# Optimization experiments

Measured on AMD Instinct MI355X. Metric: run time of the kernel, lower is better.

The kernel has to match this reference:

```python
import jax, jax.numpy as jnp
import numpy as np

DIM = 2048
HEADS = 16
HEAD_DIM = DIM // HEADS
B, S = 2, 2048


def setup_inputs() -> dict:
    key = jax.random.key(0)
    k1, k2, k3 = jax.random.split(key, 3)
    x = jax.random.normal(k1, (B, S, DIM), dtype=jnp.float32)
    # causal mask (True = keep), realistic production usage of masked_fill(mask==0,...)
    mask = jnp.tril(jnp.ones((S, S), dtype=bool))
    scale = 1.0 / np.sqrt(DIM)
    W_qkv = jax.random.normal(k2, (DIM, 3 * DIM), dtype=jnp.float32) * scale
    b_qkv = jnp.zeros((3 * DIM,), dtype=jnp.float32)
    W_out = jax.random.normal(k3, (DIM, DIM), dtype=jnp.float32) * scale
    b_out = jnp.zeros((DIM,), dtype=jnp.float32)
    return {"x": x, "mask": mask, "W_qkv": W_qkv, "b_qkv": b_qkv,
            "W_out": W_out, "b_out": b_out}


def reference(x, mask, W_qkv, b_qkv, W_out, b_out):
    b, s, d = x.shape
    # fused QKV projection: [b,s,3d]
    qkv = jnp.einsum('bsd,de->bse', x, W_qkv) + b_qkv
    # [b, s, h, 3*hd] -> [b, h, s, 3*hd] -> chunk into q,k,v
    qkv = qkv.reshape(b, s, HEADS, 3 * HEAD_DIM).transpose(0, 2, 1, 3)
    q, k, v = jnp.split(qkv, 3, axis=-1)  # each [b,h,s,hd]
    scores = jnp.einsum('bhqd,bhkd->bhqk', q, k) / np.sqrt(HEAD_DIM)
    scores = jnp.where(mask, scores, jnp.float32(-1e9))
    attn = jax.nn.softmax(scores, axis=-1)
    # dropout_rate = 0.0 (eval) -> identity
    out = jnp.einsum('bhqk,bhkd->bhqd', attn, v)  # [b,h,s,hd]
    out = out.transpose(0, 2, 1, 3).reshape(b, s, d)
    return jnp.einsum('bsd,de->bse', out, W_out) + b_out
```

## Files before the change

kernel.cpp:

```cpp
#include <hip/hip_runtime.h>
#include <hip/hip_bf16.h>

#define SEQ   2048
#define DIMSZ 2048
#define NHEAD 16
#define HD    128
#define KDIM  2048

typedef __attribute__((ext_vector_type(8))) short bf16x8;
typedef __attribute__((ext_vector_type(4))) float f32x4;
typedef __attribute__((ext_vector_type(4))) short short4v;
typedef __attribute__((ext_vector_type(4))) float float4v;

__device__ __forceinline__ short f2bf(float f) {
    union { __hip_bfloat16 h; short s; } u;
    u.h = __float2bfloat16(f);
    return u.s;
}

__device__ __forceinline__ void gload_lds16(const void* g, void* l) {
    __builtin_amdgcn_global_load_lds(
        (const __attribute__((address_space(1))) void*)g,
        (__attribute__((address_space(3))) void*)l, 16, 0, 0);
}

__global__ __launch_bounds__(256) void cvt_bf16(const float* __restrict__ in,
                                                short* __restrict__ out) {
    int i = (blockIdx.x * 256 + threadIdx.x) * 4;
    float4v v = *reinterpret_cast<const float4v*>(in + i);
    short4v o;
    o[0] = f2bf(v[0]); o[1] = f2bf(v[1]); o[2] = f2bf(v[2]); o[3] = f2bf(v[3]);
    *reinterpret_cast<short4v*>(out + i) = o;
}

__global__ __launch_bounds__(256) void transpose_cvt(const float* __restrict__ in,
                                                     short* __restrict__ out,
                                                     int R, int C) {
    __shared__ float tile[32][33];
    int c0 = blockIdx.x * 32, r0 = blockIdx.y * 32;
    int tx = threadIdx.x, ty = threadIdx.y;
#pragma unroll
    for (int i = 0; i < 32; i += 8)
        tile[ty + i][tx] = in[(long)(r0 + ty + i) * C + c0 + tx];
    __syncthreads();
#pragma unroll
    for (int i = 0; i < 32; i += 8)
        out[(long)(c0 + ty + i) * R + r0 + tx] = f2bf(tile[tx][ty + i]);
}

template <int MODE, int BM, int BN, int WMC, int WNC>
__global__ __launch_bounds__(512, 2) void gemm8p(const short* __restrict__ A,
                                                 const short* __restrict__ Bt,
                                                 const float* __restrict__ bias,
                                                 float* __restrict__ outf,
                                                 short* __restrict__ q_buf,
                                                 short* __restrict__ k_buf,
                                                 short* __restrict__ vt_buf,
                                                 int ntx) {
    constexpr int QMW = (BM / 2) / WMC;
    constexpr int QNW = (BN / 2) / WNC;
    constexpr int MA = QMW / 16;
    constexpr int NB = QNW / 16;
    constexpr int UA = BM / 64, UB = BN / 64, UT = UA + UB;
    constexpr int RA = MA * 2, RB = NB * 2;
    constexpr int BH0C = (BN / 2 + 63) / 64;
    constexpr int NE = UA / 2 + BH0C, NL = UT - NE;
    constexpr int S0 = 2, S2 = 2;
    constexpr int VM0 = NE + S0;
    constexpr int VM2 = NL + S2;
    constexpr int VM3 = (NE - S2) + NE;
    constexpr int NT = KDIM / 64;

    __shared__ __align__(16) short Alds[2][BM * 64];
    __shared__ __align__(16) short Blds[2][BN * 64];

    const int tid = threadIdx.x;
    const int wv = tid >> 6, ln = tid & 63;
    const int lr = ln & 15, lg = ln >> 4;
    const int wm = wv / WNC, wn = wv % WNC;
    const int q8 = gridDim.x >> 3;
    const int id = blockIdx.x;
    const int swz = (id & 7) * q8 + (id >> 3);
    const int m0 = (swz / ntx) * BM, n0 = (swz % ntx) * BN;

    const int r_l = wv * 8 + (ln >> 3);
    const int g8 = ((ln & 7) ^ ((ln >> 3) & 7)) << 3;

#define STAGE_U(u, bufi, TT)                                                   \
    {                                                                          \
        const bool isA_ = (u) < UA / 2 || (u) >= UA / 2 + UB;                  \
        const int idx_ = (u) < UA / 2 ? (u)                                    \
                         : ((u) < UA / 2 + UB ? (u) - UA / 2 : (u) - UB);      \
        if (isA_)                                                              \
            gload_lds16(A + (long)(m0 + idx_ * 64 + r_l) * KDIM + (TT)*64 + g8,\
                        &Alds[bufi][idx_ * 4096 + wv * 512]);                  \
        else                                                                   \
            gload_lds16(Bt + (long)(n0 + idx_ * 64 + r_l) * KDIM + (TT)*64 + g8,\
                        &Blds[bufi][idx_ * 4096 + wv * 512]);                  \
    }

#define RD(L_, row_, kk_) \
    (*reinterpret_cast<const bf16x8*>(&(L_)[(row_)*64 + ((((kk_)*4 + lg) ^ ((row_)&7)) << 3)]))

#define RD_A(bufi, mh, bank)                                                   \
    _Pragma("unroll") for (int mi = 0; mi < MA; ++mi) {                        \
        int r_ = (mh) * (BM / 2) + wm * QMW + mi * 16 + lr;                    \
        bank[mi][0] = RD(Alds[bufi], r_, 0);                                   \
        bank[mi][1] = RD(Alds[bufi], r_, 1);                                   \
    }
#define RD_B(bufi, nh, bank)                                                   \
    _Pragma("unroll") for (int ni = 0; ni < NB; ++ni) {                        \
        int r_ = (nh) * (BN / 2) + wn * QNW + ni * 16 + lr;                    \
        bank[ni][0] = RD(Blds[bufi], r_, 0);                                   \
        bank[ni][1] = RD(Blds[bufi], r_, 1);                                   \
    }

#define MFMA_Q(qi, AB, BB)                                                     \
    __builtin_amdgcn_s_setprio(1);                                             \
    _Pragma("unroll") for (int kk = 0; kk < 2; ++kk)                           \
        _Pragma("unroll") for (int mi = 0; mi < MA; ++mi)                      \
            _Pragma("unroll") for (int ni = 0; ni < NB; ++ni)                  \
                acc[qi][mi][ni] = __builtin_amdgcn_mfma_f32_16x16x32_bf16(     \
                    AB[mi][kk], BB[ni][kk], acc[qi][mi][ni], 0, 0, 0);         \
    __builtin_amdgcn_s_setprio(0);

#define LGKM(n)                                                                \
    asm volatile("s_waitcnt lgkmcnt(%0)" ::"i"(n) : "memory");                 \
    __builtin_amdgcn_sched_barrier(0);
#define VMC(n) asm volatile("s_waitcnt vmcnt(%0)" ::"i"(n) : "memory");
#define BAR()                                                                  \
    __builtin_amdgcn_s_barrier();                                              \
    __builtin_amdgcn_sched_barrier(0);

    f32x4 acc[4][MA][NB] = {};
    bf16x8 aF0[MA][2], aF1[MA][2], bF0a[NB][2], bF0b[NB][2], bF1[NB][2];

#pragma unroll
    for (int u = 0; u < UT; ++u) STAGE_U(u, 0, 0);
#pragma unroll
    for (int u = 0; u < NE; ++u) STAGE_U(u, 1, 1);
    VMC(NE);
    BAR();
    RD_A(0, 0, aF0);
    RD_B(0, 0, bF0a);

#define TILE_BODY(PAR, T_, BF0C, BF0N)                                         \
    {                                                                          \
        constexpr int cur = PAR, nxt = PAR ^ 1;                                \
                 \
        RD_B(cur, 1, bF1);                                                     \
        if ((T_) + 1 < NT) {                                                   \
            STAGE_U(NE + 0, nxt, (T_) + 1);                                    \
            STAGE_U(NE + 1, nxt, (T_) + 1);                                    \
        }                                                                      \
        LGKM(RB);                                                              \
        MFMA_Q(0, aF0, BF0C);                                                  \
        VMC(VM0);                                                              \
        BAR();                                                                 \
                \
        RD_A(cur, 1, aF1);                                                     \
        if ((T_) + 1 < NT) {                                                   \
            _Pragma("unroll") for (int u = NE + S0; u < UT; ++u)               \
                STAGE_U(u, nxt, (T_) + 1);                                     \
        }                                                                      \
        LGKM(RA);                                                              \
        MFMA_Q(1, aF0, bF1);                                                   \
        BAR();                                                                 \
                       \
        if ((T_) + 2 < NT) {                                                   \
            STAGE_U(0, cur, (T_) + 2);                                         \
            STAGE_U(1, cur, (T_) + 2);                                         \
        }                                                                      \
        LGKM(0);                                                               \
        MFMA_Q(2, aF1, bF1);                                                   \
        if ((T_) + 2 < NT) { VMC(VM2); } else { VMC(NL); }                     \
        BAR();                                                                 \
           \
        if ((T_) + 1 < NT) {                                                   \
            RD_A(nxt, 0, aF0);                                                 \
            RD_B(nxt, 0, BF0N);                                                \
        }                                                                      \
        if ((T_) + 2 < NT) {                                                   \
            _Pragma("unroll") for (int u = S2; u < NE; ++u)                    \
                STAGE_U(u, cur, (T_) + 2);                                     \
        }                                                                      \
        LGKM(RA + RB);                                                         \
        MFMA_Q(3, aF1, BF0C);                                                  \
        if ((T_) + 2 < NT) { VMC(VM3); } else { VMC(0); }                      \
        BAR();                                                                 \
    }

    for (int TT = 0; TT < NT; TT += 2) {
        TILE_BODY(0, TT, bF0a, bF0b);
        TILE_BODY(1, TT + 1, bF0b, bF0a);
    }

    const int MH[4] = {0, 0, 1, 1}, NHq[4] = {0, 1, 1, 0};
#pragma unroll
    for (int q = 0; q < 4; ++q) {
#pragma unroll
        for (int mi = 0; mi < MA; ++mi) {
#pragma unroll
            for (int ni = 0; ni < NB; ++ni) {
                int col = n0 + NHq[q] * (BN / 2) + wn * QNW + ni * 16 + lr;
                float bv = bias[col];
#pragma unroll
                for (int j = 0; j < 4; ++j) {
                    int row = m0 + MH[q] * (BM / 2) + wm * QMW + mi * 16 + lg * 4 + j;
                    float v = acc[q][mi][ni][j] + bv;
                    if (MODE == 0) {
                        int h = col / (3 * HD);
                        int jj = col - h * (3 * HD);
                        int b = row >> 11, s = row & 2047;
                        int bh = b * NHEAD + h;
                        short sv = f2bf(v);
                        if (jj < HD)
                            q_buf[(bh * SEQ + s) * HD + jj] = sv;
                        else if (jj < 2 * HD)
                            k_buf[(bh * SEQ + s) * HD + (jj - HD)] = sv;
                        else
                            vt_buf[(bh * HD + (jj - 2 * HD)) * SEQ + s] = sv;
                    } else {
                        outf[(long)row * DIMSZ + col] = v;
                    }
                }
            }
        }
    }
#undef STAGE_U
#undef RD
#undef RD_A
#undef RD_B
#undef MFMA_Q
#undef LGKM
#undef VMC
#undef BAR
#undef TILE_BODY
}

__global__ __launch_bounds__(256, 2) void attn_kernel(const short* __restrict__ q_buf,
                                                      const short* __restrict__ k_buf,
                                                      const short* __restrict__ vt_buf,
                                                      short* __restrict__ ao) {
    __shared__ __align__(16) short Klds[2][64 * 128];
    __shared__ __align__(16) short Vlds[2][128 * 64];
    __shared__ __align__(16) short Plds[4][32 * 64];
    const int tid = threadIdx.x;
    const int wave = tid >> 6, lane = tid & 63;
    const int lr = lane & 15, lg = lane >> 4;
    const int bx = blockIdx.x;
    const int qt = 15 - (bx >> 5);
    const int bh = bx & 31;
    const int b = bh >> 4, h = bh & 15;
    const int qbase = qt * 128 + wave * 32;
    const float scale = 0.08838834764831845f;

    bf16x8 qf[2][4];
    {
        const short* qrow = q_buf + ((long)(bh * SEQ + qbase + lr)) * HD;
#pragma unroll
        for (int mi = 0; mi < 2; ++mi)
#pragma unroll
            for (int c = 0; c < 4; ++c)
                qf[mi][c] = *reinterpret_cast<const bf16x8*>(
                    qrow + mi * 16 * HD + c * 32 + lg * 8);
    }
    asm volatile("s_waitcnt vmcnt(0)" ::: "memory");

    const char* kbase = (const char*)(k_buf + (long)bh * SEQ * HD);
    const char* vbase = (const char*)(vt_buf + (long)bh * HD * SEQ);
    const int krow_l = wave * 4 + (lane >> 4);
    const int kcol_l = ((lane & 15) * 16) ^ ((krow_l & 7) << 4);
    const int vrow_l = wave * 8 + (lane >> 3);
    const int vcol_l = ((lane & 7) * 16) ^ ((vrow_l & 7) << 4);

    const int nt = 2 * (qt + 1);
    auto stage = [&](int bufi, int t) {
        const char* ks = kbase + (long)t * 16384 + (long)krow_l * 256 + kcol_l;
        const char* vs = vbase + (long)t * 128 + (long)vrow_l * (SEQ * 2) + vcol_l;
        short* kd = &Klds[bufi][wave * 512];
        short* vd = &Vlds[bufi][wave * 512];
#pragma unroll
        for (int i = 0; i < 4; ++i) {
            gload_lds16(ks + i * 4096, kd + i * 2048);
            gload_lds16(vs + (long)i * 32 * SEQ * 2, vd + i * 2048);
        }
    };

    f32x4 o_acc[2][8] = {};
    float mrow[2][4], lrow[2][4];
#pragma unroll
    for (int mi = 0; mi < 2; ++mi)
#pragma unroll
        for (int j = 0; j < 4; ++j) { mrow[mi][j] = -1e30f; lrow[mi][j] = 0.f; }
    short* pw = &Plds[wave][0];

    stage(0, 0);
    for (int t = 0; t < nt; ++t) {
        const int cur = t & 1;
        if (t + 1 < nt) {
            stage(cur ^ 1, t + 1);
            asm volatile("s_waitcnt vmcnt(8)" ::: "memory");
        } else {
            asm volatile("s_waitcnt vmcnt(0)" ::: "memory");
        }
        __builtin_amdgcn_s_barrier();
        __builtin_amdgcn_sched_barrier(0);

        const int kv0 = t * 64;
        if (kv0 <= qbase + 31) {
            f32x4 sc[2][4] = {};
            const short* kl = &Klds[cur][0];
#pragma unroll
            for (int c = 0; c < 4; ++c) {
                bf16x8 kf[4];
#pragma unroll
                for (int ni = 0; ni < 4; ++ni)
                    kf[ni] = *reinterpret_cast<const bf16x8*>(
                        kl + (((ni * 16 + lr) * 256 +
                               ((c * 64 + lg * 16) ^ ((lr & 7) << 4))) >> 1));
#pragma unroll
                for (int mi = 0; mi < 2; ++mi)
#pragma unroll
                    for (int ni = 0; ni < 4; ++ni)
                        sc[mi][ni] = __builtin_amdgcn_mfma_f32_16x16x32_bf16(
                            qf[mi][c], kf[ni], sc[mi][ni], 0, 0, 0);
            }
            const bool full = (kv0 + 63) <= qbase;
            float pv[2][4][4], pm[2][4];
#pragma unroll
            for (int mi = 0; mi < 2; ++mi)
#pragma unroll
                for (int j = 0; j < 4; ++j) {
                    float mx = -3e38f;
#pragma unroll
                    for (int ni = 0; ni < 4; ++ni) {
                        float v = sc[mi][ni][j] * scale;
                        if (!full) {
                            int qg = qbase + mi * 16 + lg * 4 + j;
                            if (kv0 + ni * 16 + lr > qg) v = -1e9f;
                        }
                        pv[mi][ni][j] = v;
                        mx = fmaxf(mx, v);
                    }
                    pm[mi][j] = mx;
                }
#pragma unroll
            for (int m = 1; m < 16; m <<= 1)
#pragma unroll
                for (int mi = 0; mi < 2; ++mi)
#pragma unroll
                    for (int j = 0; j < 4; ++j)
                        pm[mi][j] = fmaxf(pm[mi][j], __shfl_xor(pm[mi][j], m, 64));
            float alpha[2][4], psum[2][4];
#pragma unroll
            for (int mi = 0; mi < 2; ++mi)
#pragma unroll
                for (int j = 0; j < 4; ++j) {
                    float mn = fmaxf(mrow[mi][j], pm[mi][j]);
                    alpha[mi][j] = __expf(mrow[mi][j] - mn);
                    mrow[mi][j] = mn;
                    psum[mi][j] = 0.f;
                }
#pragma unroll
            for (int mi = 0; mi < 2; ++mi)
#pragma unroll
                for (int ni = 0; ni < 4; ++ni)
#pragma unroll
                    for (int j = 0; j < 4; ++j) {
                        float p = __expf(pv[mi][ni][j] - mrow[mi][j]);
                        pv[mi][ni][j] = p;
                        psum[mi][j] += p;
                    }
#pragma unroll
            for (int m = 1; m < 16; m <<= 1)
#pragma unroll
                for (int mi = 0; mi < 2; ++mi)
#pragma unroll
                    for (int j = 0; j < 4; ++j)
                        psum[mi][j] += __shfl_xor(psum[mi][j], m, 64);
#pragma unroll
            for (int mi = 0; mi < 2; ++mi)
#pragma unroll
                for (int j = 0; j < 4; ++j)
                    lrow[mi][j] = lrow[mi][j] * alpha[mi][j] + psum[mi][j];
#pragma unroll
            for (int mi = 0; mi < 2; ++mi)
#pragma unroll
                for (int n = 0; n < 8; ++n)
#pragma unroll
                    for (int j = 0; j < 4; ++j)
                        o_acc[mi][n][j] *= alpha[mi][j];
#pragma unroll
            for (int mi = 0; mi < 2; ++mi)
#pragma unroll
                for (int ni = 0; ni < 4; ++ni)
#pragma unroll
                    for (int j = 0; j < 4; ++j) {
                        int row = mi * 16 + lg * 4 + j;
                        int cb = (ni * 32 + lr * 2) ^ ((row & 7) << 4);
                        pw[(row * 128 + cb) >> 1] = f2bf(pv[mi][ni][j]);
                    }
            const short* vl = &Vlds[cur][0];
#pragma unroll
            for (int kc = 0; kc < 2; ++kc) {
                bf16x8 pa[2];
#pragma unroll
                for (int mi = 0; mi < 2; ++mi)
                    pa[mi] = *reinterpret_cast<const bf16x8*>(
                        pw + (((mi * 16 + lr) * 128 +
                               ((kc * 64 + lg * 16) ^ ((lr & 7) << 4))) >> 1));
#pragma unroll
                for (int n = 0; n < 8; ++n) {
                    bf16x8 vf = *reinterpret_cast<const bf16x8*>(
                        vl + (((n * 16 + lr) * 128 +
                               ((kc * 64 + lg * 16) ^ ((lr & 7) << 4))) >> 1));
#pragma unroll
                    for (int mi = 0; mi < 2; ++mi)
                        o_acc[mi][n] = __builtin_amdgcn_mfma_f32_16x16x32_bf16(
                            pa[mi], vf, o_acc[mi][n], 0, 0, 0);
                }
            }
        }
        __builtin_amdgcn_s_barrier();
    }

    float inv[2][4];
#pragma unroll
    for (int mi = 0; mi < 2; ++mi)
#pragma unroll
        for (int j = 0; j < 4; ++j) inv[mi][j] = 1.0f / lrow[mi][j];
    short* aor = ao + ((long)(b * SEQ + qbase) * DIMSZ + h * HD);
#pragma unroll
    for (int mi = 0; mi < 2; ++mi)
#pragma unroll
        for (int n = 0; n < 8; ++n)
#pragma unroll
            for (int j = 0; j < 4; ++j)
                aor[(mi * 16 + lg * 4 + j) * DIMSZ + n * 16 + lr] =
                    f2bf(o_acc[mi][n][j] * inv[mi][j]);
}

extern "C" void kernel_launch(void* const* d_in, const int* in_sizes, int n_in,
                              void* d_out, int out_size, void* d_ws, size_t ws_size,
                              hipStream_t stream) {
    const float* x     = (const float*)d_in[0];
    const float* W_qkv = (const float*)d_in[2];
    const float* b_qkv = (const float*)d_in[3];
    const float* W_out = (const float*)d_in[4];
    const float* b_out = (const float*)d_in[5];
    float* out = (float*)d_out;

    char* ws = (char*)d_ws;
    short* x_bf   = (short*)ws;
    short* wqkv_t = (short*)(ws + (size_t)16 * 1048576);
    short* wout_t = (short*)(ws + (size_t)40 * 1048576);
    short* q_buf  = (short*)(ws + (size_t)48 * 1048576);
    short* k_buf  = (short*)(ws + (size_t)64 * 1048576);
    short* vt_buf = (short*)(ws + (size_t)80 * 1048576);
    short* ao     = x_bf;

    cvt_bf16<<<8192, 256, 0, stream>>>(x, x_bf);
    transpose_cvt<<<dim3(192, 64), dim3(32, 8), 0, stream>>>(W_qkv, wqkv_t, 2048, 6144);
    transpose_cvt<<<dim3(64, 64), dim3(32, 8), 0, stream>>>(W_out, wout_t, 2048, 2048);
    gemm8p<0, 256, 192, 4, 2><<<512, 512, 0, stream>>>(x_bf, wqkv_t, b_qkv, nullptr,
                                                       q_buf, k_buf, vt_buf, 32);
    attn_kernel<<<512, 256, 0, stream>>>(q_buf, k_buf, vt_buf, ao);
    gemm8p<1, 128, 256, 2, 4><<<256, 512, 0, stream>>>(ao, wout_t, b_out, out,
                                                       nullptr, nullptr, nullptr, 8);
}
```

Baseline: 327.8 us.

## Restructure attention into single-wave blocks reading K/V directly from global

```diff
diff --git a/kernel.cpp b/kernel.cpp
--- a/kernel.cpp
+++ b/kernel.cpp
@@ -147,7 +147,6 @@
 #define TILE_BODY(PAR, T_, BF0C, BF0N)                                         \
     {                                                                          \
         constexpr int cur = PAR, nxt = PAR ^ 1;                                \
-                 \
         RD_B(cur, 1, bF1);                                                     \
         if ((T_) + 1 < NT) {                                                   \
             STAGE_U(NE + 0, nxt, (T_) + 1);                                    \
@@ -157,7 +156,6 @@
         MFMA_Q(0, aF0, BF0C);                                                  \
         VMC(VM0);                                                              \
         BAR();                                                                 \
-                \
         RD_A(cur, 1, aF1);                                                     \
         if ((T_) + 1 < NT) {                                                   \
             _Pragma("unroll") for (int u = NE + S0; u < UT; ++u)               \
@@ -166,7 +164,6 @@
         LGKM(RA);                                                              \
         MFMA_Q(1, aF0, bF1);                                                   \
         BAR();                                                                 \
-                       \
         if ((T_) + 2 < NT) {                                                   \
             STAGE_U(0, cur, (T_) + 2);                                         \
             STAGE_U(1, cur, (T_) + 2);                                         \
@@ -175,7 +172,6 @@
         MFMA_Q(2, aF1, bF1);                                                   \
         if ((T_) + 2 < NT) { VMC(VM2); } else { VMC(NL); }                     \
         BAR();                                                                 \
-           \
         if ((T_) + 1 < NT) {                                                   \
             RD_A(nxt, 0, aF0);                                                 \
             RD_B(nxt, 0, BF0N);                                                \
@@ -238,21 +234,19 @@
 #undef TILE_BODY
 }
 
-__global__ __launch_bounds__(256, 2) void attn_kernel(const short* __restrict__ q_buf,
-                                                      const short* __restrict__ k_buf,
-                                                      const short* __restrict__ vt_buf,
-                                                      short* __restrict__ ao) {
-    __shared__ __align__(16) short Klds[2][64 * 128];
-    __shared__ __align__(16) short Vlds[2][128 * 64];
-    __shared__ __align__(16) short Plds[4][32 * 64];
-    const int tid = threadIdx.x;
-    const int wave = tid >> 6, lane = tid & 63;
+__global__ __launch_bounds__(64, 3) void attn_kernel(const short* __restrict__ q_buf,
+                                                     const short* __restrict__ k_buf,
+                                                     const short* __restrict__ vt_buf,
+                                                     short* __restrict__ ao) {
+    __shared__ __align__(16) short Plds[32 * 64];
+    const int lane = threadIdx.x;
     const int lr = lane & 15, lg = lane >> 4;
     const int bx = blockIdx.x;
-    const int qt = 15 - (bx >> 5);
-    const int bh = bx & 31;
+    const int t = (bx & 7) * 256 + (bx >> 3);
+    const int bh = t >> 6;
+    const int qt = 63 - (t & 63);
     const int b = bh >> 4, h = bh & 15;
-    const int qbase = qt * 128 + wave * 32;
+    const int qbase = qt * 32;
     const float scale = 0.08838834764831845f;
 
     bf16x8 qf[2][4];
@@ -265,27 +259,9 @@
                 qf[mi][c] = *reinterpret_cast<const bf16x8*>(
                     qrow + mi * 16 * HD + c * 32 + lg * 8);
     }
-    asm volatile("s_waitcnt vmcnt(0)" ::: "memory");
-
-    const char* kbase = (const char*)(k_buf + (long)bh * SEQ * HD);
-    const char* vbase = (const char*)(vt_buf + (long)bh * HD * SEQ);
-    const int krow_l = wave * 4 + (lane >> 4);
-    const int kcol_l = ((lane & 15) * 16) ^ ((krow_l & 7) << 4);
-    const int vrow_l = wave * 8 + (lane >> 3);
-    const int vcol_l = ((lane & 7) * 16) ^ ((vrow_l & 7) << 4);
-
-    const int nt = 2 * (qt + 1);
-    auto stage = [&](int bufi, int t) {
-        const char* ks = kbase + (long)t * 16384 + (long)krow_l * 256 + kcol_l;
-        const char* vs = vbase + (long)t * 128 + (long)vrow_l * (SEQ * 2) + vcol_l;
-        short* kd = &Klds[bufi][wave * 512];
-        short* vd = &Vlds[bufi][wave * 512];
-#pragma unroll
-        for (int i = 0; i < 4; ++i) {
-            gload_lds16(ks + i * 4096, kd + i * 2048);
-            gload_lds16(vs + (long)i * 32 * SEQ * 2, vd + i * 2048);
-        }
-    };
+
+    const short* kb = k_buf + (long)bh * SEQ * HD;
+    const short* vb = vt_buf + (long)bh * HD * SEQ;
 
     f32x4 o_acc[2][8] = {};
     float mrow[2][4], lrow[2][4];
@@ -293,136 +269,126 @@
     for (int mi = 0; mi < 2; ++mi)
 #pragma unroll
         for (int j = 0; j < 4; ++j) { mrow[mi][j] = -1e30f; lrow[mi][j] = 0.f; }
-    short* pw = &Plds[wave][0];
-
-    stage(0, 0);
-    for (int t = 0; t < nt; ++t) {
-        const int cur = t & 1;
-        if (t + 1 < nt) {
-            stage(cur ^ 1, t + 1);
-            asm volatile("s_waitcnt vmcnt(8)" ::: "memory");
-        } else {
-            asm volatile("s_waitcnt vmcnt(0)" ::: "memory");
+
+    const int nt = ((qbase + 31) >> 6) + 1;
+    for (int tt = 0; tt < nt; ++tt) {
+        const int kv0 = tt * 64;
+        f32x4 sc[2][4] = {};
+#pragma unroll
+        for (int c = 0; c < 4; ++c) {
+            bf16x8 kf[4];
+#pragma unroll
+            for (int ni = 0; ni < 4; ++ni)
+                kf[ni] = *reinterpret_cast<const bf16x8*>(
+                    kb + (long)(kv0 + ni * 16 + lr) * HD + c * 32 + lg * 8);
+            __builtin_amdgcn_s_setprio(1);
+#pragma unroll
+            for (int mi = 0; mi < 2; ++mi)
+#pragma unroll
+                for (int ni = 0; ni < 4; ++ni)
+                    sc[mi][ni] = __builtin_amdgcn_mfma_f32_16x16x32_bf16(
+                        qf[mi][c], kf[ni], sc[mi][ni], 0, 0, 0);
+            __builtin_amdgcn_s_setprio(0);
         }
-        __builtin_amdgcn_s_barrier();
-        __builtin_amdgcn_sched_barrier(0);
-
-        const int kv0 = t * 64;
-        if (kv0 <= qbase + 31) {
-            f32x4 sc[2][4] = {};
-            const short* kl = &Klds[cur][0];
-#pragma unroll
-            for (int c = 0; c < 4; ++c) {
-                bf16x8 kf[4];
-#pragma unroll
-                for (int ni = 0; ni < 4; ++ni)
-                    kf[ni] = *reinterpret_cast<const bf16x8*>(
-                        kl + (((ni * 16 + lr) * 256 +
-                               ((c * 64 + lg * 16) ^ ((lr & 7) << 4))) >> 1));
-#pragma unroll
-                for (int mi = 0; mi < 2; ++mi)
-#pragma unroll
-                    for (int ni = 0; ni < 4; ++ni)
-                        sc[mi][ni] = __builtin_amdgcn_mfma_f32_16x16x32_bf16(
-                            qf[mi][c], kf[ni], sc[mi][ni], 0, 0, 0);
+        const bool full = (kv0 + 63) <= qbase;
+        float pm[2][4];
+#pragma unroll
+        for (int mi = 0; mi < 2; ++mi)
+#pragma unroll
+            for (int j = 0; j < 4; ++j) {
+                float mx = -3e38f;
+#pragma unroll
+                for (int ni = 0; ni < 4; ++ni) {
+                    float v = sc[mi][ni][j] * scale;
+                    if (!full) {
+                        int qg = qbase + mi * 16 + lg * 4 + j;
+                        if (kv0 + ni * 16 + lr > qg) v = -1e9f;
+                    }
+                    sc[mi][ni][j] = v;
+                    mx = fmaxf(mx, v);
+                }
+                pm[mi][j] = mx;
             }
-            const bool full = (kv0 + 63) <= qbase;
-            float pv[2][4][4], pm[2][4];
+#pragma unroll
+        for (int m = 1; m < 16; m <<= 1)
 #pragma unroll
             for (int mi = 0; mi < 2; ++mi)
 #pragma unroll
-                for (int j = 0; j < 4; ++j) {
-                    float mx = -3e38f;
-#pragma unroll
-                    for (int ni = 0; ni < 4; ++ni) {
-                        float v = sc[mi][ni][j] * scale;
-                        if (!full) {
-                            int qg = qbase + mi * 16 + lg * 4 + j;
-                            if (kv0 + ni * 16 + lr > qg) v = -1e9f;
-                        }
-                        pv[mi][ni][j] = v;
-                        mx = fmaxf(mx, v);
-                    }
-                    pm[mi][j] = mx;
-                }
-#pragma unroll
-            for (int m = 1; m < 16; m <<= 1)
-#pragma unroll
-                for (int mi = 0; mi < 2; ++mi)
-#pragma unroll
-                    for (int j = 0; j < 4; ++j)
-                        pm[mi][j] = fmaxf(pm[mi][j], __shfl_xor(pm[mi][j], m, 64));
-            float alpha[2][4], psum[2][4];
+                for (int j = 0; j < 4; ++j)
+                    pm[mi][j] = fmaxf(pm[mi][j], __shfl_xor(pm[mi][j], m, 64));
+        float md = -3e38f;
+#pragma unroll
+        for (int mi = 0; mi < 2; ++mi)
+#pragma unroll
+            for (int j = 0; j < 4; ++j)
+                md = fmaxf(md, pm[mi][j] - mrow[mi][j]);
+        if (!__all(md <= 8.0f)) {
 #pragma unroll
             for (int mi = 0; mi < 2; ++mi)
 #pragma unroll
                 for (int j = 0; j < 4; ++j) {
                     float mn = fmaxf(mrow[mi][j], pm[mi][j]);
-                    alpha[mi][j] = __expf(mrow[mi][j] - mn);
+                    float a = __expf(mrow[mi][j] - mn);
                     mrow[mi][j] = mn;
-                    psum[mi][j] = 0.f;
+                    lrow[mi][j] *= a;
+#pragma unroll
+                    for (int n = 0; n < 8; ++n)
+                        o_acc[mi][n][j] *= a;
                 }
+        }
+        float psum[2][4] = {};
+#pragma unroll
+        for (int mi = 0; mi < 2; ++mi)
+#pragma unroll
+            for (int ni = 0; ni < 4; ++ni)
+#pragma unroll
+                for (int j = 0; j < 4; ++j) {
+                    float p = __expf(sc[mi][ni][j] - mrow[mi][j]);
+                    sc[mi][ni][j] = p;
+                    psum[mi][j] += p;
+                }
+#pragma unroll
+        for (int m = 1; m < 16; m <<= 1)
 #pragma unroll
             for (int mi = 0; mi < 2; ++mi)
 #pragma unroll
-                for (int ni = 0; ni < 4; ++ni)
-#pragma unroll
-                    for (int j = 0; j < 4; ++j) {
-                        float p = __expf(pv[mi][ni][j] - mrow[mi][j]);
-                        pv[mi][ni][j] = p;
-                        psum[mi][j] += p;
-                    }
-#pragma unroll
-            for (int m = 1; m < 16; m <<= 1)
+                for (int j = 0; j < 4; ++j)
+                    psum[mi][j] += __shfl_xor(psum[mi][j], m, 64);
+#pragma unroll
+        for (int mi = 0; mi < 2; ++mi)
+#pragma unroll
+            for (int j = 0; j < 4; ++j)
+                lrow[mi][j] += psum[mi][j];
+#pragma unroll
+        for (int mi = 0; mi < 2; ++mi)
+#pragma unroll
+            for (int ni = 0; ni < 4; ++ni)
+#pragma unroll
+                for (int j = 0; j < 4; ++j) {
+                    int row = mi * 16 + lg * 4 + j;
+                    int cb = (ni * 32 + lr * 2) ^ ((row & 7) << 4);
+                    Plds[(row * 128 + cb) >> 1] = f2bf(sc[mi][ni][j]);
+                }
+#pragma unroll
+        for (int kc = 0; kc < 2; ++kc) {
+            bf16x8 pa[2];
+#pragma unroll
+            for (int mi = 0; mi < 2; ++mi)
+                pa[mi] = *reinterpret_cast<const bf16x8*>(
+                    &Plds[(((mi * 16 + lr) * 128 +
+                            ((kc * 64 + lg * 16) ^ ((lr & 7) << 4))) >> 1)]);
+#pragma unroll
+            for (int n = 0; n < 8; ++n) {
+                bf16x8 vf = *reinterpret_cast<const bf16x8*>(
+                    vb + (long)(n * 16 + lr) * SEQ + kv0 + kc * 32 + lg * 8);
+                __builtin_amdgcn_s_setprio(1);
 #pragma unroll
                 for (int mi = 0; mi < 2; ++mi)
-#pragma unroll
-                    for (int j = 0; j < 4; ++j)
-                        psum[mi][j] += __shfl_xor(psum[mi][j], m, 64);
-#pragma unroll
-            for (int mi = 0; mi < 2; ++mi)
-#pragma unroll
-                for (int j = 0; j < 4; ++j)
-                    lrow[mi][j] = lrow[mi][j] * alpha[mi][j] + psum[mi][j];
-#pragma unroll
-            for (int mi = 0; mi < 2; ++mi)
-#pragma unroll
-                for (int n = 0; n < 8; ++n)
-#pragma unroll
-                    for (int j = 0; j < 4; ++j)
-                        o_acc[mi][n][j] *= alpha[mi][j];
-#pragma unroll
-            for (int mi = 0; mi < 2; ++mi)
-#pragma unroll
-                for (int ni = 0; ni < 4; ++ni)
-#pragma unroll
-                    for (int j = 0; j < 4; ++j) {
-                        int row = mi * 16 + lg * 4 + j;
-                        int cb = (ni * 32 + lr * 2) ^ ((row & 7) << 4);
-                        pw[(row * 128 + cb) >> 1] = f2bf(pv[mi][ni][j]);
-                    }
-            const short* vl = &Vlds[cur][0];
-#pragma unroll
-            for (int kc = 0; kc < 2; ++kc) {
-                bf16x8 pa[2];
-#pragma unroll
-                for (int mi = 0; mi < 2; ++mi)
-                    pa[mi] = *reinterpret_cast<const bf16x8*>(
-                        pw + (((mi * 16 + lr) * 128 +
-                               ((kc * 64 + lg * 16) ^ ((lr & 7) << 4))) >> 1));
-#pragma unroll
-                for (int n = 0; n < 8; ++n) {
-                    bf16x8 vf = *reinterpret_cast<const bf16x8*>(
-                        vl + (((n * 16 + lr) * 128 +
-                               ((kc * 64 + lg * 16) ^ ((lr & 7) << 4))) >> 1));
-#pragma unroll
-                    for (int mi = 0; mi < 2; ++mi)
-                        o_acc[mi][n] = __builtin_amdgcn_mfma_f32_16x16x32_bf16(
-                            pa[mi], vf, o_acc[mi][n], 0, 0, 0);
-                }
+                    o_acc[mi][n] = __builtin_amdgcn_mfma_f32_16x16x32_bf16(
+                        pa[mi], vf, o_acc[mi][n], 0, 0, 0);
+                __builtin_amdgcn_s_setprio(0);
             }
         }
-        __builtin_amdgcn_s_barrier();
     }
 
     float inv[2][4];
@@ -465,7 +431,7 @@
     transpose_cvt<<<dim3(64, 64), dim3(32, 8), 0, stream>>>(W_out, wout_t, 2048, 2048);
     gemm8p<0, 256, 192, 4, 2><<<512, 512, 0, stream>>>(x_bf, wqkv_t, b_qkv, nullptr,
                                                        q_buf, k_buf, vt_buf, 32);
-    attn_kernel<<<512, 256, 0, stream>>>(q_buf, k_buf, vt_buf, ao);
+    attn_kernel<<<2048, 64, 0, stream>>>(q_buf, k_buf, vt_buf, ao);
     gemm8p<1, 128, 256, 2, 4><<<256, 512, 0, stream>>>(ao, wout_t, b_out, out,
                                                        nullptr, nullptr, nullptr, 8);
 }
```

Result: slower. 557.8 us (+70.2%).

## Single-buffer K/V in attention with split staging, exp2 softmax and lazy rescale

Applied to the files above, without the earlier changes.

```diff
diff --git a/kernel.cpp b/kernel.cpp
--- a/kernel.cpp
+++ b/kernel.cpp
@@ -147,7 +147,6 @@
 #define TILE_BODY(PAR, T_, BF0C, BF0N)                                         \
     {                                                                          \
         constexpr int cur = PAR, nxt = PAR ^ 1;                                \
-                 \
         RD_B(cur, 1, bF1);                                                     \
         if ((T_) + 1 < NT) {                                                   \
             STAGE_U(NE + 0, nxt, (T_) + 1);                                    \
@@ -157,7 +156,6 @@
         MFMA_Q(0, aF0, BF0C);                                                  \
         VMC(VM0);                                                              \
         BAR();                                                                 \
-                \
         RD_A(cur, 1, aF1);                                                     \
         if ((T_) + 1 < NT) {                                                   \
             _Pragma("unroll") for (int u = NE + S0; u < UT; ++u)               \
@@ -166,7 +164,6 @@
         LGKM(RA);                                                              \
         MFMA_Q(1, aF0, bF1);                                                   \
         BAR();                                                                 \
-                       \
         if ((T_) + 2 < NT) {                                                   \
             STAGE_U(0, cur, (T_) + 2);                                         \
             STAGE_U(1, cur, (T_) + 2);                                         \
@@ -175,7 +172,6 @@
         MFMA_Q(2, aF1, bF1);                                                   \
         if ((T_) + 2 < NT) { VMC(VM2); } else { VMC(NL); }                     \
         BAR();                                                                 \
-           \
         if ((T_) + 1 < NT) {                                                   \
             RD_A(nxt, 0, aF0);                                                 \
             RD_B(nxt, 0, BF0N);                                                \
@@ -238,12 +234,12 @@
 #undef TILE_BODY
 }
 
-__global__ __launch_bounds__(256, 2) void attn_kernel(const short* __restrict__ q_buf,
+__global__ __launch_bounds__(256, 3) void attn_kernel(const short* __restrict__ q_buf,
                                                       const short* __restrict__ k_buf,
                                                       const short* __restrict__ vt_buf,
                                                       short* __restrict__ ao) {
-    __shared__ __align__(16) short Klds[2][64 * 128];
-    __shared__ __align__(16) short Vlds[2][128 * 64];
+    __shared__ __align__(16) short Klds[64 * 128];
+    __shared__ __align__(16) short Vlds[128 * 64];
     __shared__ __align__(16) short Plds[4][32 * 64];
     const int tid = threadIdx.x;
     const int wave = tid >> 6, lane = tid & 63;
@@ -253,7 +249,7 @@
     const int bh = bx & 31;
     const int b = bh >> 4, h = bh & 15;
     const int qbase = qt * 128 + wave * 32;
-    const float scale = 0.08838834764831845f;
+    const float c2 = 0.12752775f;
 
     bf16x8 qf[2][4];
     {
@@ -275,16 +271,19 @@
     const int vcol_l = ((lane & 7) * 16) ^ ((vrow_l & 7) << 4);
 
     const int nt = 2 * (qt + 1);
-    auto stage = [&](int bufi, int t) {
+    auto stageK = [&](int t) {
         const char* ks = kbase + (long)t * 16384 + (long)krow_l * 256 + kcol_l;
+        short* kd = &Klds[wave * 512];
+#pragma unroll
+        for (int i = 0; i < 4; ++i)
+            gload_lds16(ks + i * 4096, kd + i * 2048);
+    };
+    auto stageV = [&](int t) {
         const char* vs = vbase + (long)t * 128 + (long)vrow_l * (SEQ * 2) + vcol_l;
-        short* kd = &Klds[bufi][wave * 512];
-        short* vd = &Vlds[bufi][wave * 512];
-#pragma unroll
-        for (int i = 0; i < 4; ++i) {
-            gload_lds16(ks + i * 4096, kd + i * 2048);
+        short* vd = &Vlds[wave * 512];
+#pragma unroll
+        for (int i = 0; i < 4; ++i)
             gload_lds16(vs + (long)i * 32 * SEQ * 2, vd + i * 2048);
-        }
     };
 
     f32x4 o_acc[2][8] = {};
@@ -295,102 +294,120 @@
         for (int j = 0; j < 4; ++j) { mrow[mi][j] = -1e30f; lrow[mi][j] = 0.f; }
     short* pw = &Plds[wave][0];
 
-    stage(0, 0);
+    stageK(0);
+    asm volatile("s_waitcnt vmcnt(0)" ::: "memory");
+    __builtin_amdgcn_s_barrier();
+    __builtin_amdgcn_sched_barrier(0);
+    stageV(0);
+
     for (int t = 0; t < nt; ++t) {
-        const int cur = t & 1;
+        const int kv0 = t * 64;
+        const bool work = kv0 <= qbase + 31;
+        f32x4 sc[2][4] = {};
+        if (work) {
+#pragma unroll
+            for (int c = 0; c < 4; ++c) {
+                bf16x8 kf[4];
+#pragma unroll
+                for (int ni = 0; ni < 4; ++ni)
+                    kf[ni] = *reinterpret_cast<const bf16x8*>(
+                        &Klds[(((ni * 16 + lr) * 256 +
+                                ((c * 64 + lg * 16) ^ ((lr & 7) << 4))) >> 1)]);
+                __builtin_amdgcn_s_setprio(1);
+#pragma unroll
+                for (int mi = 0; mi < 2; ++mi)
+#pragma unroll
+                    for (int ni = 0; ni < 4; ++ni)
+                        sc[mi][ni] = __builtin_amdgcn_mfma_f32_16x16x32_bf16(
+                            qf[mi][c], kf[ni], sc[mi][ni], 0, 0, 0);
+                __builtin_amdgcn_s_setprio(0);
+            }
+        }
+        __builtin_amdgcn_s_barrier();
+        __builtin_amdgcn_sched_barrier(0);
+        if (t + 1 < nt) stageK(t + 1);
+
+        if (work) {
+            const bool full = (kv0 + 63) <= qbase;
+            float pm[2][4];
+#pragma unroll
+            for (int mi = 0; mi < 2; ++mi)
+#pragma unroll
+                for (int j = 0; j < 4; ++j) {
+                    float mx = -3e38f;
+#pragma unroll
+                    for (int ni = 0; ni < 4; ++ni) {
+                        float v = sc[mi][ni][j] * c2;
+                        if (!full) {
+                            int qg = qbase + mi * 16 + lg * 4 + j;
+                            if (kv0 + ni * 16 + lr > qg) v = -1e9f;
+                        }
+                        sc[mi][ni][j] = v;
+                        mx = fmaxf(mx, v);
+                    }
+                    pm[mi][j] = mx;
+                }
+#pragma unroll
+            for (int m = 1; m < 16; m <<= 1)
+#pragma unroll
+                for (int mi = 0; mi < 2; ++mi)
+#pragma unroll
+                    for (int j = 0; j < 4; ++j)
+                        pm[mi][j] = fmaxf(pm[mi][j], __shfl_xor(pm[mi][j], m, 64));
+            float md = -3e38f;
+#pragma unroll
+            for (int mi = 0; mi < 2; ++mi)
+#pragma unroll
+                for (int j = 0; j < 4; ++j)
+                    md = fmaxf(md, pm[mi][j] - mrow[mi][j]);
+            if (!__all(md <= 11.5f)) {
+#pragma unroll
+                for (int mi = 0; mi < 2; ++mi)
+#pragma unroll
+                    for (int j = 0; j < 4; ++j) {
+                        float mn = fmaxf(mrow[mi][j], pm[mi][j]);
+                        float a = exp2f(mrow[mi][j] - mn);
+                        mrow[mi][j] = mn;
+                        lrow[mi][j] *= a;
+#pragma unroll
+                        for (int n = 0; n < 8; ++n)
+                            o_acc[mi][n][j] *= a;
+                    }
+            }
+            float psum[2][4] = {};
+#pragma unroll
+            for (int mi = 0; mi < 2; ++mi)
+#pragma unroll
+                for (int ni = 0; ni < 4; ++ni)
+#pragma unroll
+                    for (int j = 0; j < 4; ++j) {
+                        float p = exp2f(sc[mi][ni][j] - mrow[mi][j]);
+                        sc[mi][ni][j] = p;
+                        psum[mi][j] += p;
+                    }
+#pragma unroll
+            for (int m = 1; m < 16; m <<= 1)
+#pragma unroll
+                for (int mi = 0; mi < 2; ++mi)
+#pragma unroll
+                    for (int j = 0; j < 4; ++j)
+                        psum[mi][j] += __shfl_xor(psum[mi][j], m, 64);
+#pragma unroll
+            for (int mi = 0; mi < 2; ++mi)
+#pragma unroll
+                for (int j = 0; j < 4; ++j)
+                    lrow[mi][j] += psum[mi][j];
+        }
+
         if (t + 1 < nt) {
-            stage(cur ^ 1, t + 1);
-            asm volatile("s_waitcnt vmcnt(8)" ::: "memory");
+            asm volatile("s_waitcnt vmcnt(4)" ::: "memory");
         } else {
             asm volatile("s_waitcnt vmcnt(0)" ::: "memory");
         }
         __builtin_amdgcn_s_barrier();
         __builtin_amdgcn_sched_barrier(0);
 
-        const int kv0 = t * 64;
-        if (kv0 <= qbase + 31) {
-            f32x4 sc[2][4] = {};
-            const short* kl = &Klds[cur][0];
-#pragma unroll
-            for (int c = 0; c < 4; ++c) {
-                bf16x8 kf[4];
-#pragma unroll
-                for (int ni = 0; ni < 4; ++ni)
-                    kf[ni] = *reinterpret_cast<const bf16x8*>(
-                        kl + (((ni * 16 + lr) * 256 +
-                               ((c * 64 + lg * 16) ^ ((lr & 7) << 4))) >> 1));
-#pragma unroll
-                for (int mi = 0; mi < 2; ++mi)
-#pragma unroll
-                    for (int ni = 0; ni < 4; ++ni)
-                        sc[mi][ni] = __builtin_amdgcn_mfma_f32_16x16x32_bf16(
-                            qf[mi][c], kf[ni], sc[mi][ni], 0, 0, 0);
-            }
-            const bool full = (kv0 + 63) <= qbase;
-            float pv[2][4][4], pm[2][4];
-#pragma unroll
-            for (int mi = 0; mi < 2; ++mi)
-#pragma unroll
-                for (int j = 0; j < 4; ++j) {
-                    float mx = -3e38f;
-#pragma unroll
-                    for (int ni = 0; ni < 4; ++ni) {
-                        float v = sc[mi][ni][j] * scale;
-                        if (!full) {
-                            int qg = qbase + mi * 16 + lg * 4 + j;
-                            if (kv0 + ni * 16 + lr > qg) v = -1e9f;
-                        }
-                        pv[mi][ni][j] = v;
-                        mx = fmaxf(mx, v);
-                    }
-                    pm[mi][j] = mx;
-                }
-#pragma unroll
-            for (int m = 1; m < 16; m <<= 1)
-#pragma unroll
-                for (int mi = 0; mi < 2; ++mi)
-#pragma unroll
-                    for (int j = 0; j < 4; ++j)
-                        pm[mi][j] = fmaxf(pm[mi][j], __shfl_xor(pm[mi][j], m, 64));
-            float alpha[2][4], psum[2][4];
-#pragma unroll
-            for (int mi = 0; mi < 2; ++mi)
-#pragma unroll
-                for (int j = 0; j < 4; ++j) {
-                    float mn = fmaxf(mrow[mi][j], pm[mi][j]);
-                    alpha[mi][j] = __expf(mrow[mi][j] - mn);
-                    mrow[mi][j] = mn;
-                    psum[mi][j] = 0.f;
-                }
-#pragma unroll
-            for (int mi = 0; mi < 2; ++mi)
-#pragma unroll
-                for (int ni = 0; ni < 4; ++ni)
-#pragma unroll
-                    for (int j = 0; j < 4; ++j) {
-                        float p = __expf(pv[mi][ni][j] - mrow[mi][j]);
-                        pv[mi][ni][j] = p;
-                        psum[mi][j] += p;
-                    }
-#pragma unroll
-            for (int m = 1; m < 16; m <<= 1)
-#pragma unroll
-                for (int mi = 0; mi < 2; ++mi)
-#pragma unroll
-                    for (int j = 0; j < 4; ++j)
-                        psum[mi][j] += __shfl_xor(psum[mi][j], m, 64);
-#pragma unroll
-            for (int mi = 0; mi < 2; ++mi)
-#pragma unroll
-                for (int j = 0; j < 4; ++j)
-                    lrow[mi][j] = lrow[mi][j] * alpha[mi][j] + psum[mi][j];
-#pragma unroll
-            for (int mi = 0; mi < 2; ++mi)
-#pragma unroll
-                for (int n = 0; n < 8; ++n)
-#pragma unroll
-                    for (int j = 0; j < 4; ++j)
-                        o_acc[mi][n][j] *= alpha[mi][j];
+        if (work) {
 #pragma unroll
             for (int mi = 0; mi < 2; ++mi)
 #pragma unroll
@@ -399,9 +416,8 @@
                     for (int j = 0; j < 4; ++j) {
                         int row = mi * 16 + lg * 4 + j;
                         int cb = (ni * 32 + lr * 2) ^ ((row & 7) << 4);
-                        pw[(row * 128 + cb) >> 1] = f2bf(pv[mi][ni][j]);
+                        pw[(row * 128 + cb) >> 1] = f2bf(sc[mi][ni][j]);
                     }
-            const short* vl = &Vlds[cur][0];
 #pragma unroll
             for (int kc = 0; kc < 2; ++kc) {
                 bf16x8 pa[2];
@@ -413,16 +429,22 @@
 #pragma unroll
                 for (int n = 0; n < 8; ++n) {
                     bf16x8 vf = *reinterpret_cast<const bf16x8*>(
-                        vl + (((n * 16 + lr) * 128 +
-                               ((kc * 64 + lg * 16) ^ ((lr & 7) << 4))) >> 1));
+                        &Vlds[(((n * 16 + lr) * 128 +
+                                ((kc * 64 + lg * 16) ^ ((lr & 7) << 4))) >> 1)]);
+                    __builtin_amdgcn_s_setprio(1);
 #pragma unroll
                     for (int mi = 0; mi < 2; ++mi)
                         o_acc[mi][n] = __builtin_amdgcn_mfma_f32_16x16x32_bf16(
                             pa[mi], vf, o_acc[mi][n], 0, 0, 0);
+                    __builtin_amdgcn_s_setprio(0);
                 }
             }
         }
+
+        asm volatile("s_waitcnt vmcnt(0)" ::: "memory");
         __builtin_amdgcn_s_barrier();
+        __builtin_amdgcn_sched_barrier(0);
+        if (t + 1 < nt) stageV(t + 1);
     }
 
     float inv[2][4];
```

Measured after the change: 501.5 us. +53.0%, slower.

## Keep attention probabilities in registers via transposed QK^T and lane shuffles

Applied to the files above, without the earlier changes.

```diff
diff --git a/kernel.cpp b/kernel.cpp
--- a/kernel.cpp
+++ b/kernel.cpp
@@ -16,6 +16,10 @@
     union { __hip_bfloat16 h; short s; } u;
     u.h = __float2bfloat16(f);
     return u.s;
+}
+
+__device__ __forceinline__ unsigned pack_bf2(float lo, float hi) {
+    return (unsigned)(unsigned short)f2bf(lo) | ((unsigned)(unsigned short)f2bf(hi) << 16);
 }
 
 __device__ __forceinline__ void gload_lds16(const void* g, void* l) {
@@ -147,7 +151,6 @@
 #define TILE_BODY(PAR, T_, BF0C, BF0N)                                         \
     {                                                                          \
         constexpr int cur = PAR, nxt = PAR ^ 1;                                \
-                 \
         RD_B(cur, 1, bF1);                                                     \
         if ((T_) + 1 < NT) {                                                   \
             STAGE_U(NE + 0, nxt, (T_) + 1);                                    \
@@ -157,7 +160,6 @@
         MFMA_Q(0, aF0, BF0C);                                                  \
         VMC(VM0);                                                              \
         BAR();                                                                 \
-                \
         RD_A(cur, 1, aF1);                                                     \
         if ((T_) + 1 < NT) {                                                   \
             _Pragma("unroll") for (int u = NE + S0; u < UT; ++u)               \
@@ -166,7 +168,6 @@
         LGKM(RA);                                                              \
         MFMA_Q(1, aF0, bF1);                                                   \
         BAR();                                                                 \
-                       \
         if ((T_) + 2 < NT) {                                                   \
             STAGE_U(0, cur, (T_) + 2);                                         \
             STAGE_U(1, cur, (T_) + 2);                                         \
@@ -175,7 +176,6 @@
         MFMA_Q(2, aF1, bF1);                                                   \
         if ((T_) + 2 < NT) { VMC(VM2); } else { VMC(NL); }                     \
         BAR();                                                                 \
-           \
         if ((T_) + 1 < NT) {                                                   \
             RD_A(nxt, 0, aF0);                                                 \
             RD_B(nxt, 0, BF0N);                                                \
@@ -244,7 +244,6 @@
                                                       short* __restrict__ ao) {
     __shared__ __align__(16) short Klds[2][64 * 128];
     __shared__ __align__(16) short Vlds[2][128 * 64];
-    __shared__ __align__(16) short Plds[4][32 * 64];
     const int tid = threadIdx.x;
     const int wave = tid >> 6, lane = tid & 63;
     const int lr = lane & 15, lg = lane >> 4;
@@ -253,7 +252,7 @@
     const int bh = bx & 31;
     const int b = bh >> 4, h = bh & 15;
     const int qbase = qt * 128 + wave * 32;
-    const float scale = 0.08838834764831845f;
+    const float c2 = 0.12752775f;
 
     bf16x8 qf[2][4];
     {
@@ -288,12 +287,11 @@
     };
 
     f32x4 o_acc[2][8] = {};
-    float mrow[2][4], lrow[2][4];
-#pragma unroll
-    for (int mi = 0; mi < 2; ++mi)
-#pragma unroll
-        for (int j = 0; j < 4; ++j) { mrow[mi][j] = -1e30f; lrow[mi][j] = 0.f; }
-    short* pw = &Plds[wave][0];
+    float mrow[2] = {-1e30f, -1e30f}, lrow[2] = {0.f, 0.f};
+
+    const int s0 = (lane & 15) | ((lane & 16) << 1);
+    const int s1 = s0 + 16;
+    const bool hi_ni = (lane & 32) != 0;
 
     stage(0, 0);
     for (int t = 0; t < nt; ++t) {
@@ -319,126 +317,123 @@
                     kf[ni] = *reinterpret_cast<const bf16x8*>(
                         kl + (((ni * 16 + lr) * 256 +
                                ((c * 64 + lg * 16) ^ ((lr & 7) << 4))) >> 1));
+                __builtin_amdgcn_s_setprio(1);
 #pragma unroll
                 for (int mi = 0; mi < 2; ++mi)
 #pragma unroll
                     for (int ni = 0; ni < 4; ++ni)
                         sc[mi][ni] = __builtin_amdgcn_mfma_f32_16x16x32_bf16(
-                            qf[mi][c], kf[ni], sc[mi][ni], 0, 0, 0);
+                            kf[ni], qf[mi][c], sc[mi][ni], 0, 0, 0);
+                __builtin_amdgcn_s_setprio(0);
             }
             const bool full = (kv0 + 63) <= qbase;
-            float pv[2][4][4], pm[2][4];
-#pragma unroll
-            for (int mi = 0; mi < 2; ++mi)
-#pragma unroll
-                for (int j = 0; j < 4; ++j) {
-                    float mx = -3e38f;
-#pragma unroll
-                    for (int ni = 0; ni < 4; ++ni) {
-                        float v = sc[mi][ni][j] * scale;
-                        if (!full) {
-                            int qg = qbase + mi * 16 + lg * 4 + j;
-                            if (kv0 + ni * 16 + lr > qg) v = -1e9f;
-                        }
+            float pv[2][4][4], mx[2];
+#pragma unroll
+            for (int mi = 0; mi < 2; ++mi) {
+                float m_ = -3e38f;
+                const int qg = qbase + mi * 16 + lr;
+#pragma unroll
+                for (int ni = 0; ni < 4; ++ni)
+#pragma unroll
+                    for (int j = 0; j < 4; ++j) {
+                        float v = sc[mi][ni][j] * c2;
+                        if (!full && (kv0 + ni * 16 + lg * 4 + j > qg)) v = -1e9f;
                         pv[mi][ni][j] = v;
-                        mx = fmaxf(mx, v);
+                        m_ = fmaxf(m_, v);
                     }
-                    pm[mi][j] = mx;
+                mx[mi] = m_;
+            }
+#pragma unroll
+            for (int mi = 0; mi < 2; ++mi) {
+                mx[mi] = fmaxf(mx[mi], __shfl_xor(mx[mi], 16, 64));
+                mx[mi] = fmaxf(mx[mi], __shfl_xor(mx[mi], 32, 64));
+            }
+            float md = fmaxf(mx[0] - mrow[0], mx[1] - mrow[1]);
+            if (!__all(md <= 11.5f)) {
+#pragma unroll
+                for (int mi = 0; mi < 2; ++mi) {
+                    float mn = fmaxf(mrow[mi], mx[mi]);
+                    float a = exp2f(mrow[mi] - mn);
+                    mrow[mi] = mn;
+                    lrow[mi] *= a;
+#pragma unroll
+                    for (int j = 0; j < 4; ++j) {
+                        float aj = __shfl(a, (lane & 48) | (lg * 4 + j), 64);
+#pragma unroll
+                        for (int n = 0; n < 8; ++n)
+                            o_acc[mi][n][j] *= aj;
+                    }
                 }
-#pragma unroll
-            for (int m = 1; m < 16; m <<= 1)
-#pragma unroll
-                for (int mi = 0; mi < 2; ++mi)
-#pragma unroll
-                    for (int j = 0; j < 4; ++j)
-                        pm[mi][j] = fmaxf(pm[mi][j], __shfl_xor(pm[mi][j], m, 64));
-            float alpha[2][4], psum[2][4];
-#pragma unroll
-            for (int mi = 0; mi < 2; ++mi)
-#pragma unroll
-                for (int j = 0; j < 4; ++j) {
-                    float mn = fmaxf(mrow[mi][j], pm[mi][j]);
-                    alpha[mi][j] = __expf(mrow[mi][j] - mn);
-                    mrow[mi][j] = mn;
-                    psum[mi][j] = 0.f;
+            }
+            unsigned pk[2][4][2];
+#pragma unroll
+            for (int mi = 0; mi < 2; ++mi) {
+                float ps = 0.f;
+#pragma unroll
+                for (int ni = 0; ni < 4; ++ni) {
+#pragma unroll
+                    for (int j = 0; j < 4; ++j) {
+                        float p = exp2f(pv[mi][ni][j] - mrow[mi]);
+                        pv[mi][ni][j] = p;
+                        ps += p;
+                    }
+                    pk[mi][ni][0] = pack_bf2(pv[mi][ni][0], pv[mi][ni][1]);
+                    pk[mi][ni][1] = pack_bf2(pv[mi][ni][2], pv[mi][ni][3]);
                 }
-#pragma unroll
-            for (int mi = 0; mi < 2; ++mi)
-#pragma unroll
-                for (int ni = 0; ni < 4; ++ni)
-#pragma unroll
-                    for (int j = 0; j < 4; ++j) {
-                        float p = __expf(pv[mi][ni][j] - mrow[mi][j]);
-                        pv[mi][ni][j] = p;
-                        psum[mi][j] += p;
-                    }
-#pragma unroll
-            for (int m = 1; m < 16; m <<= 1)
-#pragma unroll
-                for (int mi = 0; mi < 2; ++mi)
-#pragma unroll
-                    for (int j = 0; j < 4; ++j)
-                        psum[mi][j] += __shfl_xor(psum[mi][j], m, 64);
-#pragma unroll
-            for (int mi = 0; mi < 2; ++mi)
-#pragma unroll
-                for (int j = 0; j < 4; ++j)
-                    lrow[mi][j] = lrow[mi][j] * alpha[mi][j] + psum[mi][j];
-#pragma unroll
-            for (int mi = 0; mi < 2; ++mi)
-#pragma unroll
-                for (int n = 0; n < 8; ++n)
-#pragma unroll
-                    for (int j = 0; j < 4; ++j)
-                        o_acc[mi][n][j] *= alpha[mi][j];
-#pragma unroll
-            for (int mi = 0; mi < 2; ++mi)
-#pragma unroll
-                for (int ni = 0; ni < 4; ++ni)
-#pragma unroll
-                    for (int j = 0; j < 4; ++j) {
-                        int row = mi * 16 + lg * 4 + j;
-                        int cb = (ni * 32 + lr * 2) ^ ((row & 7) << 4);
-                        pw[(row * 128 + cb) >> 1] = f2bf(pv[mi][ni][j]);
-                    }
+                ps += __shfl_xor(ps, 16, 64);
+                ps += __shfl_xor(ps, 32, 64);
+                lrow[mi] += ps;
+            }
             const short* vl = &Vlds[cur][0];
 #pragma unroll
             for (int kc = 0; kc < 2; ++kc) {
-                bf16x8 pa[2];
-#pragma unroll
-                for (int mi = 0; mi < 2; ++mi)
-                    pa[mi] = *reinterpret_cast<const bf16x8*>(
-                        pw + (((mi * 16 + lr) * 128 +
-                               ((kc * 64 + lg * 16) ^ ((lr & 7) << 4))) >> 1));
+                union { int i[4]; bf16x8 v; } pa[2];
+#pragma unroll
+                for (int mi = 0; mi < 2; ++mi) {
+                    int a0 = __shfl((int)pk[mi][2 * kc][0], s0, 64);
+                    int b0 = __shfl((int)pk[mi][2 * kc + 1][0], s0, 64);
+                    int a1 = __shfl((int)pk[mi][2 * kc][1], s0, 64);
+                    int b1 = __shfl((int)pk[mi][2 * kc + 1][1], s0, 64);
+                    int a2 = __shfl((int)pk[mi][2 * kc][0], s1, 64);
+                    int b2 = __shfl((int)pk[mi][2 * kc + 1][0], s1, 64);
+                    int a3 = __shfl((int)pk[mi][2 * kc][1], s1, 64);
+                    int b3 = __shfl((int)pk[mi][2 * kc + 1][1], s1, 64);
+                    pa[mi].i[0] = hi_ni ? b0 : a0;
+                    pa[mi].i[1] = hi_ni ? b1 : a1;
+                    pa[mi].i[2] = hi_ni ? b2 : a2;
+                    pa[mi].i[3] = hi_ni ? b3 : a3;
+                }
 #pragma unroll
                 for (int n = 0; n < 8; ++n) {
                     bf16x8 vf = *reinterpret_cast<const bf16x8*>(
                         vl + (((n * 16 + lr) * 128 +
                                ((kc * 64 + lg * 16) ^ ((lr & 7) << 4))) >> 1));
+                    __builtin_amdgcn_s_setprio(1);
 #pragma unroll
                     for (int mi = 0; mi < 2; ++mi)
                         o_acc[mi][n] = __builtin_amdgcn_mfma_f32_16x16x32_bf16(
-                            pa[mi], vf, o_acc[mi][n], 0, 0, 0);
+                            pa[mi].v, vf, o_acc[mi][n], 0, 0, 0);
+                    __builtin_amdgcn_s_setprio(0);
                 }
             }
         }
         __builtin_amdgcn_s_barrier();
     }
 
-    float inv[2][4];
+    float invq[2];
+#pragma unroll
+    for (int mi = 0; mi < 2; ++mi) invq[mi] = 1.0f / lrow[mi];
+    short* aor = ao + ((long)(b * SEQ + qbase) * DIMSZ + h * HD);
 #pragma unroll
     for (int mi = 0; mi < 2; ++mi)
 #pragma unroll
-        for (int j = 0; j < 4; ++j) inv[mi][j] = 1.0f / lrow[mi][j];
-    short* aor = ao + ((long)(b * SEQ + qbase) * DIMSZ + h * HD);
-#pragma unroll
-    for (int mi = 0; mi < 2; ++mi)
-#pragma unroll
-        for (int n = 0; n < 8; ++n)
-#pragma unroll
-            for (int j = 0; j < 4; ++j)
+        for (int j = 0; j < 4; ++j) {
+            float ij = __shfl(invq[mi], (lane & 48) | (lg * 4 + j), 64);
+#pragma unroll
+            for (int n = 0; n < 8; ++n)
                 aor[(mi * 16 + lg * 4 + j) * DIMSZ + n * 16 + lr] =
-                    f2bf(o_acc[mi][n][j] * inv[mi][j]);
+                    f2bf(o_acc[mi][n][j] * ij);
+        }
 }
 
 extern "C" void kernel_launch(void* const* d_in, const int* in_sizes, int n_in,
```

New measurement: 299.8 us. 8.5% less time.
